# Kernel optimization log

Measured on AMD Instinct MI355X. Metric: run time of the kernel, lower is better.

The kernel has to match this reference:

```python
import jax, jax.numpy as jnp
import numpy as np

# dims: B=32 batch, F=40 max_frames, NB=36 num_boxes, R=512 region size, H=512 hidden
# feat_size D = R + 2H = 1536 ; relation attn input = 2D = 3072

def _soft_attention(feats, hidden, Wf, bf, Wh, bh, wa):
    # feats: (N, L, Din), hidden: (N, H) -> att feat (N, Din), alpha (N, L)
    e = jnp.tanh(feats @ Wf.T + bf + (hidden @ Wh.T + bh)[:, None, :]) @ wa  # (N, L)
    alpha = jax.nn.softmax(e, axis=1)
    att = jnp.einsum('nl,nld->nd', alpha, feats)
    return att, alpha


def setup_inputs() -> dict:
    key = jax.random.key(0)
    ks = jax.random.split(key, 16)
    B, F, NB, R, H = 32, 40, 36, 512, 512
    D = R + 2 * H  # 1536
    s = 0.02
    inp = {
        'i3d_feats': jax.random.normal(ks[0], (B, F, 2 * H), jnp.float32),
        'object_feats': jax.random.normal(ks[1], (B, F, NB, R), jnp.float32),
        'hidden_state': jax.random.normal(ks[2], (B, H), jnp.float32),
        # spatial SoftAttention(R, H, H)
        'Ws_f': jax.random.normal(ks[3], (H, R), jnp.float32) * s,
        'bs_f': jnp.zeros((H,), jnp.float32),
        'Ws_h': jax.random.normal(ks[4], (H, H), jnp.float32) * s,
        'bs_h': jnp.zeros((H,), jnp.float32),
        'was': jax.random.normal(ks[5], (H,), jnp.float32) * s,
        # relation SoftAttention(2D, H, H)
        'Wr_f': jax.random.normal(ks[6], (H, 2 * D), jnp.float32) * s,
        'br_f': jnp.zeros((H,), jnp.float32),
        'Wr_h': jax.random.normal(ks[7], (H, H), jnp.float32) * s,
        'br_h': jnp.zeros((H,), jnp.float32),
        'war': jax.random.normal(ks[8], (H,), jnp.float32) * s,
    }
    return inp


def reference(i3d_feats, object_feats, hidden_state,
              Ws_f, bs_f, Ws_h, bs_h, was,
              Wr_f, br_f, Wr_h, br_h, war):
    B, F, NB, R = object_feats.shape
    # ---- spatial attention over boxes (per frame) ----
    feats = object_feats.reshape(B * F, NB, R)
    hidden_rep = jnp.repeat(hidden_state, F, axis=0)  # == hidden.repeat(1,F).reshape(B*F,-1)
    obj_att, _ = _soft_attention(feats, hidden_rep, Ws_f, bs_f, Ws_h, bs_h, was)
    obj_att = obj_att.reshape(B, F, R)
    feat = jnp.concatenate([obj_att, i3d_feats], axis=-1)  # (B, F, D)
    D = feat.shape[-1]
    # ---- relation attention over all F*F frame pairs ----
    # pairwise[b, i*F + j] = concat(feat[b, j], feat[b, i])  (feat1 varies fast, feat2 slow)
    # Decompose Wr_f @ concat(fj, fi) = Wr1 @ fj + Wr2 @ fi to avoid O(F^2 * 2D) tensor.
    Wr1, Wr2 = Wr_f[:, :D], Wr_f[:, D:]
    p1 = feat @ Wr1.T  # (B, F, H), applied to fast index j
    p2 = feat @ Wr2.T  # (B, F, H), applied to slow index i
    hproj = hidden_state @ Wr_h.T + br_h  # (B, H)
    e = jnp.tanh(p2[:, :, None, :] + p1[:, None, :, :] + (hproj + br_f)[:, None, None, :]) @ war  # (B,F,F) [i,j]
    alpha = jax.nn.softmax(e.reshape(B, F * F), axis=1).reshape(B, F, F)
    # weighted sum of concat(feat[j], feat[i]) splits into two marginal sums
    rel1 = jnp.einsum('bij,bjd->bd', alpha, feat)
    rel2 = jnp.einsum('bij,bid->bd', alpha, feat)
    return jnp.concatenate([rel1, rel2], axis=-1)  # (B, 2D)
```

## Files before the change

kernel.cpp:

```cpp
#include <hip/hip_runtime.h>
#include <stdint.h>

#define B_SZ 32
#define F_SZ 40
#define NB_SZ 36
#define R_SZ 512
#define H_SZ 512
#define D_SZ 1536
#define M1 (B_SZ * F_SZ * NB_SZ)
#define NROW (B_SZ * F_SZ)
#define FNB (F_SZ * NB_SZ)

typedef __attribute__((ext_vector_type(8))) short short8;
typedef __attribute__((ext_vector_type(4))) float f32x4;

__device__ __forceinline__ unsigned short f2bf(float f) {
    unsigned int x = __float_as_uint(f);
    return (unsigned short)((x + 0x7fffu + ((x >> 16) & 1u)) >> 16);
}
__device__ __forceinline__ float bf2f(unsigned short u) {
    union { unsigned int i; float f; } v; v.i = ((unsigned int)u) << 16; return v.f;
}
__device__ __forceinline__ unsigned int cvtpk(float lo, float hi) {
    unsigned int r;
    asm("v_cvt_pk_bf16_f32 %0, %1, %2" : "=v"(r) : "v"(lo), "v"(hi));
    return r;
}
__device__ __forceinline__ float fast_rcp(float x) {
    float r; asm("v_rcp_f32 %0, %1" : "=v"(r) : "v"(x)); return r;
}
__device__ __forceinline__ float fast_tanh(float x) {
    float t = __builtin_amdgcn_exp2f(2.8853900817779268f * x);
    return 1.0f - 2.0f * fast_rcp(t + 1.0f);
}

__device__ __forceinline__ void gload_lds16(const void* gsrc, void* ldst) {
    __builtin_amdgcn_global_load_lds(
        (const __attribute__((address_space(1))) unsigned int*)gsrc,
        (__attribute__((address_space(3))) unsigned int*)ldst, 16, 0, 0);
}

__global__ __launch_bounds__(256) void k_pre(
    const float* __restrict__ hidden,
    const float* __restrict__ Wsh, const float* __restrict__ bsh,
    const float* __restrict__ bsf,
    const float* __restrict__ Wrh, const float* __restrict__ brh,
    const float* __restrict__ brf,
    float* __restrict__ hs, float* __restrict__ hr,
    const float* __restrict__ Wsf, unsigned short* __restrict__ Wsb)
{
    const int t = threadIdx.x;
    if (blockIdx.x >= 256) {
        int i = ((blockIdx.x - 256) * 256 + t) * 8;
        float4 f0 = *(const float4*)(Wsf + i);
        float4 f1 = *(const float4*)(Wsf + i + 4);
        uint4 pk = {cvtpk(f0.x, f0.y), cvtpk(f0.z, f0.w),
                    cvtpk(f1.x, f1.y), cvtpk(f1.z, f1.w)};
        *(uint4*)(Wsb + i) = pk;
        return;
    }
    __shared__ float hid[H_SZ];
    const int b = blockIdx.x >> 3, hc = blockIdx.x & 7;
    for (int i = t; i < H_SZ; i += 256) hid[i] = hidden[b * H_SZ + i];
    __syncthreads();
    const int h = hc * 64 + (t >> 2), kq = t & 3;
    const float* r1 = Wsh + (size_t)h * H_SZ + kq * 128;
    const float* r2 = Wrh + (size_t)h * H_SZ + kq * 128;
    const float* hh = hid + kq * 128;
    float a1 = 0.f, a2 = 0.f;
    for (int k = 0; k < 128; k += 4) {
        float4 v1 = *(const float4*)(r1 + k);
        float4 v2 = *(const float4*)(r2 + k);
        a1 += hh[k] * v1.x + hh[k+1] * v1.y + hh[k+2] * v1.z + hh[k+3] * v1.w;
        a2 += hh[k] * v2.x + hh[k+1] * v2.y + hh[k+2] * v2.z + hh[k+3] * v2.w;
    }
    a1 += __shfl_xor(a1, 1); a1 += __shfl_xor(a1, 2);
    a2 += __shfl_xor(a2, 1); a2 += __shfl_xor(a2, 2);
    if (kq == 0) {
        hs[b * H_SZ + h] = a1 + bsh[h] + bsf[h];
        hr[b * H_SZ + h] = a2 + brh[h] + brf[h];
    }
}

__global__ __launch_bounds__(256) void k_e1_mfma(
    const float* __restrict__ feats,
    const unsigned short* __restrict__ Wsb,
    const float* __restrict__ was,
    const float* __restrict__ hs,
    float* __restrict__ e1p)
{
    __shared__ __align__(16) unsigned char As[128 * 128];
    __shared__ __align__(16) unsigned char Bs[2][128 * 128];
    __shared__ float hsl[2 * 128];
    __shared__ float wasl[128];
    __shared__ float eps[2][128];

    const int bx = blockIdx.x;
    const int wid = (bx & 7) * 180 + (bx >> 3);
    const int mb = wid >> 2, by = wid & 3;
    const int m0 = mb * 128, hb = by * 128;
    const int t = threadIdx.x;
    const int b0 = m0 / FNB, b1 = (m0 + 127) / FNB;
    const int thr = (b0 + 1) * FNB - m0;

    if (t < 128) {
        hsl[t]       = hs[b0 * H_SZ + hb + t];
        hsl[128 + t] = hs[b1 * H_SZ + hb + t];
        wasl[t]      = was[hb + t];
    }

    const int lane = t & 63, w = t >> 6;
    const int wr = w >> 1, wc = w & 1;
    const int l15 = lane & 15, lk = lane >> 4;

    int ar[4], brw[4];
#pragma unroll
    for (int i = 0; i < 4; i++) {
        ar[i]  = wr * 64 + i * 16 + l15;
        brw[i] = wc * 64 + i * 16 + l15;
    }

    const int srow = t >> 3;
    const int scol = t & 7;
    const int wub  = (t & 192) * 16;

    float4 alo[4], ahi[4];
    f32x4 acc[4][4] = {};
    float ep[4][4] = {{0.f}};

#define E1_LOAD_A(K0) do { \
    _Pragma("unroll") \
    for (int it = 0; it < 4; it++) { \
        int r = it * 32 + srow; \
        const float* src = feats + (size_t)(m0 + r) * R_SZ + (K0) + scol * 8; \
        alo[it] = *(const float4*)src; \
        ahi[it] = *(const float4*)(src + 4); \
    } } while (0)

#define E1_STAGE_B(BUF, K0) do { \
    _Pragma("unroll") \
    for (int it = 0; it < 4; it++) { \
        int r = it * 32 + srow; \
        int gc = scol ^ (r & 7); \
        gload_lds16(Wsb + (size_t)(hb + r) * R_SZ + (K0) + gc * 8, \
                    &Bs[BUF][it * 4096 + wub]); \
    } } while (0)

#define E1_WRITE_A() do { \
    _Pragma("unroll") \
    for (int it = 0; it < 4; it++) { \
        int r = it * 32 + srow; \
        uint4 pk = {cvtpk(alo[it].x, alo[it].y), cvtpk(alo[it].z, alo[it].w), \
                    cvtpk(ahi[it].x, ahi[it].y), cvtpk(ahi[it].z, ahi[it].w)}; \
        *(uint4*)(&As[r * 128 + ((scol ^ (r & 7)) << 4)]) = pk; \
    } } while (0)

#define E1_COMPUTE(BUF) do { \
    _Pragma("unroll") \
    for (int ks = 0; ks < 2; ks++) { \
        short8 a[4], bv[4]; \
        int c = ks * 4 + lk; \
        _Pragma("unroll") \
        for (int i = 0; i < 4; i++) { \
            a[i]  = *(const short8*)(&As[ar[i] * 128 + ((c ^ (ar[i] & 7)) << 4)]); \
            bv[i] = *(const short8*)(&Bs[BUF][brw[i] * 128 + ((c ^ (brw[i] & 7)) << 4)]); \
        } \
        _Pragma("unroll") \
        for (int i = 0; i < 4; i++) \
        _Pragma("unroll") \
        for (int j = 0; j < 4; j++) \
            acc[i][j] = __builtin_amdgcn_mfma_f32_16x16x32_bf16(a[i], bv[j], acc[i][j], 0, 0, 0); \
    } } while (0)

    E1_LOAD_A(0);
    E1_STAGE_B(0, 0);
    E1_WRITE_A();
    __syncthreads();

#pragma unroll
    for (int ki = 0; ki < 8; ki++) {
        const int cur = ki & 1;
        if (ki < 7) {
            E1_LOAD_A((ki + 1) * 64);
            E1_STAGE_B(cur ^ 1, (ki + 1) * 64);
        }
        E1_COMPUTE(cur);
        __syncthreads();
        if (ki < 7) {
            E1_WRITE_A();
            __syncthreads();
        }
    }

#pragma unroll
    for (int j = 0; j < 4; j++) {
        int hl = wc * 64 + j * 16 + l15;
        float wv = wasl[hl];
#pragma unroll
        for (int i = 0; i < 4; i++) {
#pragma unroll
            for (int q = 0; q < 4; q++) {
                int r = wr * 64 + i * 16 + lk * 4 + q;
                float hv = hsl[(r >= thr ? 128 : 0) + hl];
                ep[i][q] += fast_tanh(acc[i][j][q] + hv) * wv;
            }
        }
    }
#pragma unroll
    for (int i = 0; i < 4; i++)
#pragma unroll
        for (int q = 0; q < 4; q++) {
            float v = ep[i][q];
            v += __shfl_xor(v, 1);
            v += __shfl_xor(v, 2);
            v += __shfl_xor(v, 4);
            v += __shfl_xor(v, 8);
            if (l15 == 0) eps[wc][wr * 64 + i * 16 + lk * 4 + q] = v;
        }
    __syncthreads();
    if (t < 128) e1p[(size_t)by * M1 + m0 + t] = eps[0][t] + eps[1][t];
#undef E1_LOAD_A
#undef E1_STAGE_B
#undef E1_WRITE_A
#undef E1_COMPUTE
}

__global__ __launch_bounds__(256) void k_softatt(
    const float* __restrict__ feats,
    const float* __restrict__ i3d,
    const float* __restrict__ e1p,
    unsigned short* __restrict__ feat)
{
    __shared__ float alpha[NB_SZ];
    const int n = blockIdx.x, t = threadIdx.x;
    if (t < 64) {
        float v = -1e30f;
        if (t < NB_SZ) {
            int idx = n * NB_SZ + t;
            v = e1p[idx] + e1p[M1 + idx] + e1p[2 * M1 + idx] + e1p[3 * M1 + idx];
        }
        float m = v;
#pragma unroll
        for (int off = 32; off; off >>= 1) m = fmaxf(m, __shfl_xor(m, off));
        float ex = (t < NB_SZ) ? expf(v - m) : 0.f;
        float ssum = ex;
#pragma unroll
        for (int off = 32; off; off >>= 1) ssum += __shfl_xor(ssum, off);
        if (t < NB_SZ) alpha[t] = ex / ssum;
    }
    __syncthreads();

    float a0 = 0.f, a1 = 0.f;
    const float* base = feats + (size_t)n * NB_SZ * R_SZ;
    for (int ll = 0; ll < NB_SZ; ll++) {
        float al = alpha[ll];
        float2 pv = *(const float2*)(base + ll * R_SZ + 2 * t);
        a0 += al * pv.x;
        a1 += al * pv.y;
    }
    feat[(size_t)n * D_SZ + 2 * t]     = f2bf(a0);
    feat[(size_t)n * D_SZ + 2 * t + 1] = f2bf(a1);
    float4 iv = *(const float4*)(i3d + (size_t)n * 1024 + t * 4);
    unsigned short o[4] = {f2bf(iv.x), f2bf(iv.y), f2bf(iv.z), f2bf(iv.w)};
    *(uint2*)(feat + (size_t)n * D_SZ + 512 + t * 4) = *(const uint2*)o;
}

__global__ __launch_bounds__(256) void k_pgemm_mfma(
    const unsigned short* __restrict__ feat,
    const float* __restrict__ Wrf,
    float* __restrict__ p)
{
    __shared__ __align__(16) unsigned char As[2][32 * 256];
    __shared__ __align__(16) unsigned char Bs[2][32 * 256];

    const int bx = blockIdx.x;
    const int wid = (bx & 7) * 160 + (bx >> 3);
    const int mb = wid % 40, nb = wid / 40;
    const int m0 = mb * 32, j0 = nb * 32;
    const int t = threadIdx.x;

    const int lane = t & 63, w = t >> 6;
    const int wrm = w >> 1, wcn = w & 1;
    const int l15 = lane & 15, lk = lane >> 4;

    const int arow = wrm * 16 + l15;
    const int brow = wcn * 16 + l15;

    const size_t brow_base = (j0 < 512) ? (size_t)j0 * 3072
                                        : ((size_t)(j0 - 512) * 3072 + 1536);

    float4 blo[2], bhi[2];
    f32x4 acc = {};

#define PG_STAGE_A(BUF, K0) do { \
    _Pragma("unroll") \
    for (int it = 0; it < 2; it++) { \
        int cid = it * 256 + t; \
        int r = cid >> 4, c = cid & 15; \
        int gc = c ^ (r & 7); \
        gload_lds16(feat + (size_t)(m0 + r) * D_SZ + (K0) + gc * 8, \
                    &As[BUF][it * 4096 + (t & 192) * 16]); \
    } } while (0)

#define PG_LOAD_B(K0) do { \
    _Pragma("unroll") \
    for (int it = 0; it < 2; it++) { \
        int cid = it * 256 + t; \
        int r = cid >> 4, c = cid & 15; \
        const float* src = Wrf + brow_base + (size_t)r * 3072 + (K0) + c * 8; \
        blo[it] = *(const float4*)src; \
        bhi[it] = *(const float4*)(src + 4); \
    } } while (0)

#define PG_WRITE_B(BUF) do { \
    _Pragma("unroll") \
    for (int it = 0; it < 2; it++) { \
        int cid = it * 256 + t; \
        int r = cid >> 4, c = cid & 15; \
        uint4 pk = {cvtpk(blo[it].x, blo[it].y), cvtpk(blo[it].z, blo[it].w), \
                    cvtpk(bhi[it].x, bhi[it].y), cvtpk(bhi[it].z, bhi[it].w)}; \
        *(uint4*)(&Bs[BUF][r * 256 + ((c ^ (r & 7)) << 4)]) = pk; \
    } } while (0)

#define PG_COMPUTE(BUF) do { \
    _Pragma("unroll") \
    for (int ks = 0; ks < 4; ks++) { \
        int c = ks * 4 + lk; \
        short8 av = *(const short8*)(&As[BUF][arow * 256 + ((c ^ (arow & 7)) << 4)]); \
        short8 bv = *(const short8*)(&Bs[BUF][brow * 256 + ((c ^ (brow & 7)) << 4)]); \
        acc = __builtin_amdgcn_mfma_f32_16x16x32_bf16(av, bv, acc, 0, 0, 0); \
    } } while (0)

    PG_LOAD_B(0);
    PG_STAGE_A(0, 0);
    PG_WRITE_B(0);
    __syncthreads();

#pragma unroll
    for (int ki = 0; ki < 12; ki++) {
        const int cur = ki & 1;
        if (ki < 11) {
            PG_LOAD_B((ki + 1) * 128);
            PG_STAGE_A(cur ^ 1, (ki + 1) * 128);
        }
        PG_COMPUTE(cur);
        if (ki < 11) PG_WRITE_B(cur ^ 1);
        __syncthreads();
    }

#pragma unroll
    for (int q = 0; q < 4; q++) {
        int row = m0 + wrm * 16 + lk * 4 + q;
        int col = j0 + wcn * 16 + l15;
        p[(size_t)row * 1024 + col] = acc[q];
    }
#undef PG_STAGE_A
#undef PG_LOAD_B
#undef PG_WRITE_B
#undef PG_COMPUTE
}

__global__ __launch_bounds__(512) void k_e2(
    const float* __restrict__ p,
    const float* __restrict__ hr,
    const float* __restrict__ war,
    float* __restrict__ e2)
{
    __shared__ float p1l[F_SZ][512];
    const int blk = blockIdx.x;
    const int b = blk / 5, io = blk % 5;
    const int t = threadIdx.x;
    const int w = t >> 6, l = t & 63;

    for (int cid = t; cid < F_SZ * 64; cid += 512) {
        int r = cid >> 6, c = cid & 63;
        const float* src = p + (size_t)(b * F_SZ + r) * 1024 + c * 8;
        *(float4*)&p1l[r][c * 8]     = *(const float4*)src;
        *(float4*)&p1l[r][c * 8 + 4] = *(const float4*)(src + 4);
    }

    const int i = io * 8 + w;
    const int ni = b * F_SZ + i;
    float base[8], warf[8];
    {
        float4 pa = *(const float4*)(p + (size_t)ni * 1024 + 512 + l * 8);
        float4 pb = *(const float4*)(p + (size_t)ni * 1024 + 512 + l * 8 + 4);
        float4 ha = *(const float4*)(hr + b * H_SZ + l * 8);
        float4 hb = *(const float4*)(hr + b * H_SZ + l * 8 + 4);
        base[0] = pa.x + ha.x; base[1] = pa.y + ha.y; base[2] = pa.z + ha.z; base[3] = pa.w + ha.w;
        base[4] = pb.x + hb.x; base[5] = pb.y + hb.y; base[6] = pb.z + hb.z; base[7] = pb.w + hb.w;
        float4 wa = *(const float4*)(war + l * 8);
        float4 wb = *(const float4*)(war + l * 8 + 4);
        warf[0] = wa.x; warf[1] = wa.y; warf[2] = wa.z; warf[3] = wa.w;
        warf[4] = wb.x; warf[5] = wb.y; warf[6] = wb.z; warf[7] = wb.w;
    }
    __syncthreads();

    for (int j = 0; j < F_SZ; j++) {
        const float* r = p1l[j];
        float4 va = *(const float4*)(r + l * 8);
        float4 vb = *(const float4*)(r + l * 8 + 4);
        float pv[8] = {va.x, va.y, va.z, va.w, vb.x, vb.y, vb.z, vb.w};
        float s = 0.f;
#pragma unroll
        for (int u = 0; u < 8; u++) s += fast_tanh(pv[u] + base[u]) * warf[u];
#pragma unroll
        for (int off = 32; off; off >>= 1) s += __shfl_xor(s, off);
        if (l == 0) e2[(size_t)b * 1600 + i * F_SZ + j] = s;
    }
}

__global__ __launch_bounds__(256) void k_out(
    const float* __restrict__ e2,
    const unsigned short* __restrict__ feat,
    float* __restrict__ out)
{
    __shared__ float alpha[1600];
    __shared__ float red[4];
    __shared__ float rs[F_SZ], cs[F_SZ];
    const int b = blockIdx.x >> 1, half = blockIdx.x & 1;
    const int t = threadIdx.x;
    const int w = t >> 6, l = t & 63;

    float lm = -1e30f;
    for (int idx = t; idx < 1600; idx += 256) {
        float v = e2[(size_t)b * 1600 + idx];
        alpha[idx] = v;
        lm = fmaxf(lm, v);
    }
#pragma unroll
    for (int off = 32; off; off >>= 1) lm = fmaxf(lm, __shfl_xor(lm, off));
    if (l == 0) red[w] = lm;
    __syncthreads();
    float M = fmaxf(fmaxf(red[0], red[1]), fmaxf(red[2], red[3]));
    __syncthreads();
    float ls = 0.f;
    for (int idx = t; idx < 1600; idx += 256) {
        float ex = expf(alpha[idx] - M);
        alpha[idx] = ex;
        ls += ex;
    }
#pragma unroll
    for (int off = 32; off; off >>= 1) ls += __shfl_xor(ls, off);
    if (l == 0) red[w] = ls;
    __syncthreads();
    float inv = 1.f / (red[0] + red[1] + red[2] + red[3]);

    if (t < F_SZ) {
        float s = 0.f;
        for (int j = 0; j < F_SZ; j++) s += alpha[t * F_SZ + j];
        rs[t] = s * inv;
    } else if (t >= 128 && t < 128 + F_SZ) {
        int j = t - 128;
        float s = 0.f;
        for (int i2 = 0; i2 < F_SZ; i2++) s += alpha[i2 * F_SZ + j];
        cs[j] = s * inv;
    }
    __syncthreads();

    const int cb = half * 768;
    float a1[3] = {0.f, 0.f, 0.f};
    float a2[3] = {0.f, 0.f, 0.f};
    for (int r = 0; r < F_SZ; r++) {
        float w1 = cs[r], w2 = rs[r];
        const unsigned short* fr = feat + (size_t)(b * F_SZ + r) * D_SZ + cb;
#pragma unroll
        for (int u = 0; u < 3; u++) {
            float f = bf2f(fr[t + u * 256]);
            a1[u] += w1 * f;
            a2[u] += w2 * f;
        }
    }
#pragma unroll
    for (int u = 0; u < 3; u++) {
        out[(size_t)b * 3072 + cb + t + u * 256]        = a1[u];
        out[(size_t)b * 3072 + 1536 + cb + t + u * 256] = a2[u];
    }
}

extern "C" void kernel_launch(void* const* d_in, const int* in_sizes, int n_in,
                              void* d_out, int out_size, void* d_ws, size_t ws_size,
                              hipStream_t stream) {
    const float* i3d    = (const float*)d_in[0];
    const float* objf   = (const float*)d_in[1];
    const float* hidden = (const float*)d_in[2];
    const float* Wsf    = (const float*)d_in[3];
    const float* bsf    = (const float*)d_in[4];
    const float* Wsh    = (const float*)d_in[5];
    const float* bsh    = (const float*)d_in[6];
    const float* was    = (const float*)d_in[7];
    const float* Wrf    = (const float*)d_in[8];
    const float* brf    = (const float*)d_in[9];
    const float* Wrh    = (const float*)d_in[10];
    const float* brh    = (const float*)d_in[11];
    const float* war    = (const float*)d_in[12];
    float* out = (float*)d_out;

    char* ws = (char*)d_ws;
    float* hs  = (float*)(ws);
    float* hr  = (float*)(ws + 65536);
    float* p   = (float*)(ws + 131072);
    float* e1p = (float*)(ws + 131072);
    unsigned short* Wsb = (unsigned short*)(ws + 4849664);
    float* e2  = (float*)(ws + 5373952);
    unsigned short* feat = (unsigned short*)(ws + 5578752);

    k_pre<<<dim3(384), dim3(256), 0, stream>>>(hidden, Wsh, bsh, bsf, Wrh, brh, brf, hs, hr, Wsf, Wsb);
    k_e1_mfma<<<dim3(1440), dim3(256), 0, stream>>>(objf, Wsb, was, hs, e1p);
    k_softatt<<<dim3(NROW), dim3(256), 0, stream>>>(objf, i3d, e1p, feat);
    k_pgemm_mfma<<<dim3(1280), dim3(256), 0, stream>>>(feat, Wrf, p);
    k_e2<<<dim3(160), dim3(512), 0, stream>>>(p, hr, war, e2);
    k_out<<<dim3(64), dim3(256), 0, stream>>>(e2, feat, out);
}
```

Baseline: 288.0 us.

## Retile spatial-attention GEMM to 64x256 and widen softatt/e2 work per thread

The e1 MFMA kernel now uses 64-row by 256-column tiles, so each A tile of object features is converted once and reused across two 128-wide halves of the weight matrix. A and B staging are interleaved across the halves, and only two partial-energy slices need summing instead of four. This cuts redundant fp32 reads and bf16 conversion of the large object_feats tensor. k_softatt now handles two frames per block with float4 loads and packed conversion, k_e2 moves to 256-thread blocks with twice as many blocks, and expf is replaced with __expf. Risks are higher register use under the launch-bounds occupancy hint and slightly lower exp precision.

```diff
diff --git a/kernel.cpp b/kernel.cpp
--- a/kernel.cpp
+++ b/kernel.cpp
@@ -82,132 +82,132 @@
     }
 }
 
-__global__ __launch_bounds__(256) void k_e1_mfma(
+__global__ __launch_bounds__(256, 3) void k_e1_mfma(
     const float* __restrict__ feats,
     const unsigned short* __restrict__ Wsb,
     const float* __restrict__ was,
     const float* __restrict__ hs,
     float* __restrict__ e1p)
 {
-    __shared__ __align__(16) unsigned char As[128 * 128];
+    __shared__ __align__(16) unsigned char As[2][64 * 128];
     __shared__ __align__(16) unsigned char Bs[2][128 * 128];
-    __shared__ float hsl[2 * 128];
-    __shared__ float wasl[128];
-    __shared__ float eps[2][128];
+    __shared__ float hsl[2][256];
+    __shared__ float wasl[256];
+    __shared__ float eps[2][64];
 
     const int bx = blockIdx.x;
     const int wid = (bx & 7) * 180 + (bx >> 3);
-    const int mb = wid >> 2, by = wid & 3;
-    const int m0 = mb * 128, hb = by * 128;
+    const int mb = wid >> 1, by = wid & 1;
+    const int m0 = mb * 64, hb = by * 256;
     const int t = threadIdx.x;
-    const int b0 = m0 / FNB, b1 = (m0 + 127) / FNB;
+    const int b0 = m0 / FNB, b1 = (m0 + 63) / FNB;
     const int thr = (b0 + 1) * FNB - m0;
 
-    if (t < 128) {
-        hsl[t]       = hs[b0 * H_SZ + hb + t];
-        hsl[128 + t] = hs[b1 * H_SZ + hb + t];
-        wasl[t]      = was[hb + t];
+    if (t < 256) {
+        hsl[0][t] = hs[b0 * H_SZ + hb + t];
+        hsl[1][t] = hs[b1 * H_SZ + hb + t];
+        wasl[t]   = was[hb + t];
     }
 
     const int lane = t & 63, w = t >> 6;
     const int wr = w >> 1, wc = w & 1;
     const int l15 = lane & 15, lk = lane >> 4;
 
-    int ar[4], brw[4];
-#pragma unroll
-    for (int i = 0; i < 4; i++) {
-        ar[i]  = wr * 64 + i * 16 + l15;
-        brw[i] = wc * 64 + i * 16 + l15;
-    }
+    int ar[2], brw[4];
+#pragma unroll
+    for (int i = 0; i < 2; i++) ar[i] = wr * 32 + i * 16 + l15;
+#pragma unroll
+    for (int j = 0; j < 4; j++) brw[j] = wc * 64 + j * 16 + l15;
 
     const int srow = t >> 3;
     const int scol = t & 7;
     const int wub  = (t & 192) * 16;
 
-    float4 alo[4], ahi[4];
-    f32x4 acc[4][4] = {};
-    float ep[4][4] = {{0.f}};
+    float4 alo[2], ahi[2];
+    f32x4 acc[2][8] = {};
+    float ep[2][4] = {{0.f}};
 
 #define E1_LOAD_A(K0) do { \
     _Pragma("unroll") \
-    for (int it = 0; it < 4; it++) { \
-        int r = it * 32 + srow; \
-        const float* src = feats + (size_t)(m0 + r) * R_SZ + (K0) + scol * 8; \
+    for (int it = 0; it < 2; it++) { \
+        int cid = it * 256 + t; \
+        int r = cid >> 3, c = cid & 7; \
+        const float* src = feats + (size_t)(m0 + r) * R_SZ + (K0) + c * 8; \
         alo[it] = *(const float4*)src; \
         ahi[it] = *(const float4*)(src + 4); \
     } } while (0)
 
-#define E1_STAGE_B(BUF, K0) do { \
+#define E1_WRITE_A(AB) do { \
+    _Pragma("unroll") \
+    for (int it = 0; it < 2; it++) { \
+        int cid = it * 256 + t; \
+        int r = cid >> 3, c = cid & 7; \
+        uint4 pk = {cvtpk(alo[it].x, alo[it].y), cvtpk(alo[it].z, alo[it].w), \
+                    cvtpk(ahi[it].x, ahi[it].y), cvtpk(ahi[it].z, ahi[it].w)}; \
+        *(uint4*)(&As[AB][r * 128 + ((c ^ (r & 7)) << 4)]) = pk; \
+    } } while (0)
+
+#define E1_STAGE_B(BUF, HP, K0) do { \
     _Pragma("unroll") \
     for (int it = 0; it < 4; it++) { \
         int r = it * 32 + srow; \
         int gc = scol ^ (r & 7); \
-        gload_lds16(Wsb + (size_t)(hb + r) * R_SZ + (K0) + gc * 8, \
+        gload_lds16(Wsb + (size_t)(hb + (HP) * 128 + r) * R_SZ + (K0) + gc * 8, \
                     &Bs[BUF][it * 4096 + wub]); \
     } } while (0)
 
-#define E1_WRITE_A() do { \
-    _Pragma("unroll") \
-    for (int it = 0; it < 4; it++) { \
-        int r = it * 32 + srow; \
-        uint4 pk = {cvtpk(alo[it].x, alo[it].y), cvtpk(alo[it].z, alo[it].w), \
-                    cvtpk(ahi[it].x, ahi[it].y), cvtpk(ahi[it].z, ahi[it].w)}; \
-        *(uint4*)(&As[r * 128 + ((scol ^ (r & 7)) << 4)]) = pk; \
-    } } while (0)
-
-#define E1_COMPUTE(BUF) do { \
+#define E1_COMPUTE(HP, BB, AB) do { \
     _Pragma("unroll") \
     for (int ks = 0; ks < 2; ks++) { \
-        short8 a[4], bv[4]; \
+        short8 a[2], bv[4]; \
         int c = ks * 4 + lk; \
         _Pragma("unroll") \
-        for (int i = 0; i < 4; i++) { \
-            a[i]  = *(const short8*)(&As[ar[i] * 128 + ((c ^ (ar[i] & 7)) << 4)]); \
-            bv[i] = *(const short8*)(&Bs[BUF][brw[i] * 128 + ((c ^ (brw[i] & 7)) << 4)]); \
-        } \
-        _Pragma("unroll") \
-        for (int i = 0; i < 4; i++) \
+        for (int i = 0; i < 2; i++) \
+            a[i] = *(const short8*)(&As[AB][ar[i] * 128 + ((c ^ (ar[i] & 7)) << 4)]); \
         _Pragma("unroll") \
         for (int j = 0; j < 4; j++) \
-            acc[i][j] = __builtin_amdgcn_mfma_f32_16x16x32_bf16(a[i], bv[j], acc[i][j], 0, 0, 0); \
+            bv[j] = *(const short8*)(&Bs[BB][brw[j] * 128 + ((c ^ (brw[j] & 7)) << 4)]); \
+        _Pragma("unroll") \
+        for (int i = 0; i < 2; i++) \
+        _Pragma("unroll") \
+        for (int j = 0; j < 4; j++) \
+            acc[i][(HP) * 4 + j] = __builtin_amdgcn_mfma_f32_16x16x32_bf16( \
+                a[i], bv[j], acc[i][(HP) * 4 + j], 0, 0, 0); \
     } } while (0)
 
     E1_LOAD_A(0);
-    E1_STAGE_B(0, 0);
-    E1_WRITE_A();
-    __syncthreads();
-
-#pragma unroll
+    E1_STAGE_B(0, 0, 0);
+    E1_WRITE_A(0);
+    __syncthreads();
+
     for (int ki = 0; ki < 8; ki++) {
-        const int cur = ki & 1;
-        if (ki < 7) {
-            E1_LOAD_A((ki + 1) * 64);
-            E1_STAGE_B(cur ^ 1, (ki + 1) * 64);
-        }
-        E1_COMPUTE(cur);
+        const int ab = ki & 1;
+        E1_STAGE_B(1, 1, ki * 64);
+        if (ki < 7) E1_LOAD_A((ki + 1) * 64);
+        E1_COMPUTE(0, 0, ab);
         __syncthreads();
-        if (ki < 7) {
-            E1_WRITE_A();
-            __syncthreads();
-        }
-    }
-
-#pragma unroll
-    for (int j = 0; j < 4; j++) {
-        int hl = wc * 64 + j * 16 + l15;
+        if (ki < 7) E1_STAGE_B(0, 0, (ki + 1) * 64);
+        E1_COMPUTE(1, 1, ab);
+        if (ki < 7) E1_WRITE_A(ab ^ 1);
+        __syncthreads();
+    }
+
+#pragma unroll
+    for (int jj = 0; jj < 8; jj++) {
+        int hl = (jj >> 2) * 128 + wc * 64 + (jj & 3) * 16 + l15;
         float wv = wasl[hl];
 #pragma unroll
-        for (int i = 0; i < 4; i++) {
+        for (int i = 0; i < 2; i++) {
 #pragma unroll
             for (int q = 0; q < 4; q++) {
-                int r = wr * 64 + i * 16 + lk * 4 + q;
-                float hv = hsl[(r >= thr ? 128 : 0) + hl];
-                ep[i][q] += fast_tanh(acc[i][j][q] + hv) * wv;
+                int r = wr * 32 + i * 16 + lk * 4 + q;
+                float hv = hsl[r >= thr ? 1 : 0][hl];
+                ep[i][q] += fast_tanh(acc[i][jj][q] + hv) * wv;
             }
         }
     }
 #pragma unroll
-    for (int i = 0; i < 4; i++)
+    for (int i = 0; i < 2; i++)
 #pragma unroll
         for (int q = 0; q < 4; q++) {
             float v = ep[i][q];
@@ -215,13 +215,13 @@
             v += __shfl_xor(v, 2);
             v += __shfl_xor(v, 4);
             v += __shfl_xor(v, 8);
-            if (l15 == 0) eps[wc][wr * 64 + i * 16 + lk * 4 + q] = v;
+            if (l15 == 0) eps[wc][wr * 32 + i * 16 + lk * 4 + q] = v;
         }
     __syncthreads();
-    if (t < 128) e1p[(size_t)by * M1 + m0 + t] = eps[0][t] + eps[1][t];
+    if (t < 64) e1p[(size_t)by * M1 + m0 + t] = eps[0][t] + eps[1][t];
 #undef E1_LOAD_A
+#undef E1_WRITE_A
 #undef E1_STAGE_B
-#undef E1_WRITE_A
 #undef E1_COMPUTE
 }
 
@@ -231,38 +231,48 @@
     const float* __restrict__ e1p,
     unsigned short* __restrict__ feat)
 {
-    __shared__ float alpha[NB_SZ];
-    const int n = blockIdx.x, t = threadIdx.x;
-    if (t < 64) {
+    __shared__ float alpha[2][NB_SZ];
+    const int n0 = blockIdx.x * 2;
+    const int t = threadIdx.x;
+    const int w = t >> 6;
+
+    if (w < 2) {
+        const int n = n0 + w, lane = t & 63;
         float v = -1e30f;
-        if (t < NB_SZ) {
-            int idx = n * NB_SZ + t;
-            v = e1p[idx] + e1p[M1 + idx] + e1p[2 * M1 + idx] + e1p[3 * M1 + idx];
+        if (lane < NB_SZ) {
+            int idx = n * NB_SZ + lane;
+            v = e1p[idx] + e1p[M1 + idx];
         }
         float m = v;
 #pragma unroll
         for (int off = 32; off; off >>= 1) m = fmaxf(m, __shfl_xor(m, off));
-        float ex = (t < NB_SZ) ? expf(v - m) : 0.f;
+        float ex = (lane < NB_SZ) ? __expf(v - m) : 0.f;
         float ssum = ex;
 #pragma unroll
         for (int off = 32; off; off >>= 1) ssum += __shfl_xor(ssum, off);
-        if (t < NB_SZ) alpha[t] = ex / ssum;
-    }
-    __syncthreads();
-
-    float a0 = 0.f, a1 = 0.f;
-    const float* base = feats + (size_t)n * NB_SZ * R_SZ;
+        if (lane < NB_SZ) alpha[w][lane] = ex / ssum;
+    }
+    __syncthreads();
+
+    const int g = t >> 7, lc = t & 127;
+    const int n = n0 + g;
+    float4 a4 = {0.f, 0.f, 0.f, 0.f};
+    const float* base = feats + (size_t)n * NB_SZ * R_SZ + lc * 4;
     for (int ll = 0; ll < NB_SZ; ll++) {
-        float al = alpha[ll];
-        float2 pv = *(const float2*)(base + ll * R_SZ + 2 * t);
-        a0 += al * pv.x;
-        a1 += al * pv.y;
-    }
-    feat[(size_t)n * D_SZ + 2 * t]     = f2bf(a0);
-    feat[(size_t)n * D_SZ + 2 * t + 1] = f2bf(a1);
-    float4 iv = *(const float4*)(i3d + (size_t)n * 1024 + t * 4);
-    unsigned short o[4] = {f2bf(iv.x), f2bf(iv.y), f2bf(iv.z), f2bf(iv.w)};
-    *(uint2*)(feat + (size_t)n * D_SZ + 512 + t * 4) = *(const uint2*)o;
+        float al = alpha[g][ll];
+        float4 pv = *(const float4*)(base + ll * R_SZ);
+        a4.x += al * pv.x; a4.y += al * pv.y;
+        a4.z += al * pv.z; a4.w += al * pv.w;
+    }
+    uint2 att = {cvtpk(a4.x, a4.y), cvtpk(a4.z, a4.w)};
+    *(uint2*)(feat + (size_t)n * D_SZ + lc * 4) = att;
+
+    const float* ib = i3d + (size_t)n * 1024 + lc * 8;
+    float4 iv0 = *(const float4*)ib;
+    float4 iv1 = *(const float4*)(ib + 4);
+    uint4 pk = {cvtpk(iv0.x, iv0.y), cvtpk(iv0.z, iv0.w),
+                cvtpk(iv1.x, iv1.y), cvtpk(iv1.z, iv1.w)};
+    *(uint4*)(feat + (size_t)n * D_SZ + 512 + lc * 8) = pk;
 }
 
 __global__ __launch_bounds__(256) void k_pgemm_mfma(
@@ -360,7 +370,7 @@
 #undef PG_COMPUTE
 }
 
-__global__ __launch_bounds__(512) void k_e2(
+__global__ __launch_bounds__(256) void k_e2(
     const float* __restrict__ p,
     const float* __restrict__ hr,
     const float* __restrict__ war,
@@ -368,18 +378,20 @@
 {
     __shared__ float p1l[F_SZ][512];
     const int blk = blockIdx.x;
-    const int b = blk / 5, io = blk % 5;
+    const int b = blk / 10, io = blk % 10;
     const int t = threadIdx.x;
     const int w = t >> 6, l = t & 63;
 
-    for (int cid = t; cid < F_SZ * 64; cid += 512) {
+#pragma unroll
+    for (int u = 0; u < 10; u++) {
+        int cid = u * 256 + t;
         int r = cid >> 6, c = cid & 63;
         const float* src = p + (size_t)(b * F_SZ + r) * 1024 + c * 8;
         *(float4*)&p1l[r][c * 8]     = *(const float4*)src;
         *(float4*)&p1l[r][c * 8 + 4] = *(const float4*)(src + 4);
     }
 
-    const int i = io * 8 + w;
+    const int i = io * 4 + w;
     const int ni = b * F_SZ + i;
     float base[8], warf[8];
     {
@@ -436,7 +448,7 @@
     __syncthreads();
     float ls = 0.f;
     for (int idx = t; idx < 1600; idx += 256) {
-        float ex = expf(alpha[idx] - M);
+        float ex = __expf(alpha[idx] - M);
         alpha[idx] = ex;
         ls += ex;
     }
@@ -507,8 +519,8 @@
 
     k_pre<<<dim3(384), dim3(256), 0, stream>>>(hidden, Wsh, bsh, bsf, Wrh, brh, brf, hs, hr, Wsf, Wsb);
     k_e1_mfma<<<dim3(1440), dim3(256), 0, stream>>>(objf, Wsb, was, hs, e1p);
-    k_softatt<<<dim3(NROW), dim3(256), 0, stream>>>(objf, i3d, e1p, feat);
+    k_softatt<<<dim3(640), dim3(256), 0, stream>>>(objf, i3d, e1p, feat);
     k_pgemm_mfma<<<dim3(1280), dim3(256), 0, stream>>>(feat, Wrf, p);
-    k_e2<<<dim3(160), dim3(512), 0, stream>>>(p, hr, war, e2);
+    k_e2<<<dim3(320), dim3(256), 0, stream>>>(p, hr, war, e2);
     k_out<<<dim3(64), dim3(256), 0, stream>>>(e2, feat, out);
 }
```

Result: faster. 273.5 us (-5.0%).
